# Kernel tuning notes

Hardware: AMD Instinct MI355X
Metric: run time of the kernel (lower is better)

The kernel has to match this reference:

```python
import jax, jax.numpy as jnp
import numpy as np

PENALTY_LAMBDA = 0.5
MAX_RULES = 512
INIT_GATE_LOGIT = -2.0


def setup_inputs() -> dict:
    key = jax.random.key(0)
    k1, k2, k3 = jax.random.split(key, 3)
    B, V, E = 64, 128000, 1000000
    logits = jax.random.normal(k1, (B, V), dtype=jnp.float32)
    # learned per-rule gate logits (nn.Parameter initialized at init_gate_logit;
    # we perturb slightly so gradients are non-degenerate)
    gate_logits = jnp.full((MAX_RULES,), INIT_GATE_LOGIT, dtype=jnp.float32) \
        + 0.1 * jax.random.normal(k2, (MAX_RULES,), dtype=jnp.float32)
    # flattened ragged (rule, token) violation pairs
    kr, kt = jax.random.split(k3)
    rule_ids = jax.random.randint(kr, (E,), 0, MAX_RULES, dtype=jnp.int32)
    token_ids = jax.random.randint(kt, (E,), 0, V, dtype=jnp.int32)
    return {"logits": logits, "gate_logits": gate_logits,
            "rule_ids": rule_ids, "token_ids": token_ids}


def reference(logits, gate_logits, rule_ids, token_ids):
    # eval-mode binary concrete gate (no noise, no thresholding): sigmoid(logit)
    gates = jax.nn.sigmoid(gate_logits)                      # [R]
    V = logits.shape[-1]
    # gated penalty value per (rule, token) pair, single vectorized scatter-add
    vals = gates[rule_ids] * jnp.asarray(PENALTY_LAMBDA, logits.dtype)  # [E]
    pen_1d = jnp.zeros((V,), dtype=logits.dtype).at[token_ids].add(vals)  # [V]
    penalties = jnp.broadcast_to(pen_1d[None, :], logits.shape)           # [B,V]
    modified = logits - penalties
    # coverage loss: -mean of gates over rules that fire (have >=1 violation)
    firing = jnp.zeros((MAX_RULES,), dtype=logits.dtype).at[rule_ids].set(1.0)
    n_firing = jnp.maximum(firing.sum(), 1.0)
    coverage_loss = -(gates * firing).sum() / n_firing
    return modified, coverage_loss, penalties
```

## Files before the change

### kernel.cpp

```cpp
#include <hip/hip_runtime.h>

#define PENALTY_LAMBDA 0.5f
#define RULES 512
#define NR 4
#define RS 32000
#define VOCAB 128000
#define G 64
#define NB 64
#define CH 500
#define CJ 125

typedef float    f32x4 __attribute__((ext_vector_type(4)));
typedef _Float16 f16x4 __attribute__((ext_vector_type(4)));


__global__ void __launch_bounds__(512) scatter_kernel(
    const int* __restrict__ rule_ids, const int* __restrict__ token_ids,
    const float* __restrict__ gate_logits, _Float16* __restrict__ partials,
    unsigned* __restrict__ masks, int E) {
    __shared__ __align__(16) float hist[RS];
    __shared__ float s_g[RULES];
    __shared__ unsigned char s_f[RULES];
    int t = threadIdx.x;
    int g = blockIdx.x;
    int r = blockIdx.y;
    for (int i = t * 4; i < RS; i += 512 * 4)
        *(f32x4*)(hist + i) = (f32x4){0.f, 0.f, 0.f, 0.f};
    if (t < RULES) {
        float x = gate_logits[t];
        s_g[t] = PENALTY_LAMBDA / (1.0f + expf(-x));
    }
    if (t < RULES / 4) ((unsigned*)s_f)[t] = 0u;
    __syncthreads();

    const int lo = r * RS;
    const int stride = G * 512 * 4;
    for (int base = (g * 512 + t) * 4; base + 4 <= E; base += stride) {
        int4 tt = *(const int4*)(token_ids + base);
        int4 rr = *(const int4*)(rule_ids + base);
        int ts[4] = {tt.x, tt.y, tt.z, tt.w};
        int rv[4] = {rr.x, rr.y, rr.z, rr.w};
#pragma unroll
        for (int k = 0; k < 4; ++k) {
            int tok = ts[k] - lo;
            if ((unsigned)tok < (unsigned)RS) atomicAdd(&hist[tok], s_g[rv[k]]);
            if (r == 0) s_f[rv[k]] = 1;
        }
    }
    if (g == 0 && t == 0) {
        for (int e = E & ~3; e < E; ++e) {
            int tok = token_ids[e] - lo; int ru = rule_ids[e];
            if ((unsigned)tok < (unsigned)RS) atomicAdd(&hist[tok], s_g[ru]);
            if (r == 0) s_f[ru] = 1;
        }
    }
    __syncthreads();

    _Float16* dst = partials + ((size_t)r * G + g) * RS;
    for (int i = t * 4; i < RS; i += 512 * 4) {
        f32x4 s = *(const f32x4*)(&hist[i]);
        f16x4 h = {(_Float16)s.x, (_Float16)s.y, (_Float16)s.z, (_Float16)s.w};
        *(f16x4*)(dst + i) = h;
    }

    if (r == 0 && t < 16) {
        const unsigned* w = (const unsigned*)s_f + t * 8;
        unsigned m = 0;
#pragma unroll
        for (int k = 0; k < 8; ++k) {
            unsigned d = w[k];
            if (d & 0x000000FFu) m |= 1u << (k * 4 + 0);
            if (d & 0x0000FF00u) m |= 1u << (k * 4 + 1);
            if (d & 0x00FF0000u) m |= 1u << (k * 4 + 2);
            if (d & 0xFF000000u) m |= 1u << (k * 4 + 3);
        }
        masks[g * 16 + t] = m;
    }
}

__global__ void __launch_bounds__(512) fused_kernel(
    const _Float16* __restrict__ partials, const unsigned* __restrict__ masks,
    const float* __restrict__ gate_logits, const float* __restrict__ logits,
    float* __restrict__ out_mod, float* __restrict__ out_pen,
    float* __restrict__ out_loss) {
    __shared__ float s_pc[CH + 4];
    __shared__ f32x4 s_part[4][CJ + 1];
    int t = threadIdx.x;
    int tx = t & 127, ty = t >> 7;
    int chunk = blockIdx.x;
    int c0 = chunk * CH;
    int r = c0 / RS;
    int bin = c0 - r * RS;

    {
        if (tx < CJ) {
            f32x4 acc = {0.f, 0.f, 0.f, 0.f};
            const _Float16* bp = partials + ((size_t)r * G + ty * 16) * RS
                               + bin + tx * 4;
#pragma unroll 4
            for (int g = 0; g < 16; ++g) {
                f16x4 h = *(const f16x4*)(bp + (size_t)g * RS);
                acc += (f32x4){(float)h.x, (float)h.y, (float)h.z, (float)h.w};
            }
            s_part[ty][tx] = acc;
        } else if (tx == 127) {
            f32x4 e = {0.f, 0.f, 0.f, 0.f};
            for (int i = 0; i < 4; ++i) {
                int gb = c0 + CH + i; if (gb >= VOCAB) gb -= VOCAB;
                int r2 = gb / RS, b2 = gb - r2 * RS;
                const _Float16* bp2 = partials + ((size_t)r2 * G + ty * 16) * RS + b2;
                float s = 0.f;
                for (int g = 0; g < 16; ++g) s += (float)bp2[(size_t)g * RS];
                ((float*)&e)[i] = s;
            }
            s_part[ty][CJ] = e;
        }
    }
    __syncthreads();
    if (t < CJ + 1) {
        f32x4 s = s_part[0][t] + s_part[1][t] + s_part[2][t] + s_part[3][t];
        *(f32x4*)(s_pc + t * 4) = s;
    }
    __syncthreads();

    if (chunk == 0) {
        __shared__ unsigned s_mask[16];
        __shared__ float sg[8], sf[8];
        if (t < 16) {
            unsigned m = 0;
            for (int g = 0; g < G; ++g) m |= masks[g * 16 + t];
            s_mask[t] = m;
        }
        __syncthreads();
        float f = ((s_mask[t >> 5] >> (t & 31)) & 1u) ? 1.f : 0.f;
        float gf = f / (1.f + expf(-gate_logits[t]));
        for (int off = 32; off > 0; off >>= 1) {
            gf += __shfl_down(gf, off, 64);
            f  += __shfl_down(f,  off, 64);
        }
        if ((t & 63) == 0) { sg[t >> 6] = gf; sf[t >> 6] = f; }
        __syncthreads();
        if (t == 0) {
            float tg = 0.f, tf = 0.f;
            for (int w = 0; w < 8; ++w) { tg += sg[w]; tf += sf[w]; }
            *out_loss = -tg / fmaxf(tf, 1.0f);
            out_pen[0] = s_pc[0];
            out_pen[1] = s_pc[1];
            out_pen[2] = s_pc[2];
        }
    }

    if (tx >= CJ) return;
    f32x4 p0 = *(const f32x4*)(s_pc + tx * 4);
    f32x4 ps = {s_pc[tx * 4 + 3], s_pc[tx * 4 + 4],
                s_pc[tx * 4 + 5], s_pc[tx * 4 + 6]};
    bool glast = (chunk == 255 && tx == CJ - 1);
    size_t col = (size_t)c0 + tx * 4;
#pragma unroll 4
    for (int ib = 0; ib < NB / 4; ++ib) {
        int b = ib * 4 + ty;
        size_t base = (size_t)b * VOCAB + col;
        f32x4 l = *(const f32x4*)(logits + base);
        *(f32x4*)(out_mod + base) = l - p0;
        if (glast && b == NB - 1) {
            out_pen[base + 3] = p0.w;
        } else {
            *(f32x4*)(out_pen + base + 3) = ps;
        }
    }
}

extern "C" void kernel_launch(void* const* d_in, const int* in_sizes, int n_in,
                              void* d_out, int out_size, void* d_ws, size_t ws_size,
                              hipStream_t stream) {
    const float* logits      = (const float*)d_in[0];
    const float* gate_logits = (const float*)d_in[1];
    const int*   rule_ids    = (const int*)d_in[2];
    const int*   token_ids   = (const int*)d_in[3];
    float* out = (float*)d_out;

    const int E = in_sizes[2];
    const size_t BV = (size_t)NB * VOCAB;

    _Float16* partials = (_Float16*)d_ws;
    unsigned* masks    = (unsigned*)(partials + (size_t)NR * G * RS);

    scatter_kernel<<<dim3(G, NR), 512, 0, stream>>>(
        rule_ids, token_ids, gate_logits, partials, masks, E);

    fused_kernel<<<VOCAB / CH, 512, 0, stream>>>(
        partials, masks, gate_logits, logits,
        out, out + BV + 1, out + BV);
}
```

Before: 117.9 us.

## Replace per-block LDS histograms with global float atomics into one penalty vector

The partitioned shared-memory histograms and fp16 partial buffers are removed. Instead, a small init kernel zeroes a single 128K-float penalty vector and precomputes the gates, and the scatter kernel applies unsafe (hardware) float atomics straight to that global vector. Rule-firing masks are merged with atomicOr. The fused kernel now reads only the final penalty row, runs on a 2D grid, and uses nontemporal loads and stores. This removes the 32 MB partial write/read and the multi-pass reduction, at the cost of heavy global atomic contention, an extra kernel launch, and a summation order that is no longer deterministic.

New measurement: 160.8 us. 36.4% more time.

```diff
diff --git a/kernel.cpp b/kernel.cpp
--- a/kernel.cpp
+++ b/kernel.cpp
@@ -1,69 +1,56 @@
 #include <hip/hip_runtime.h>
 
-#define PENALTY_LAMBDA 0.5f
 #define RULES 512
-#define NR 4
-#define RS 32000
 #define VOCAB 128000
-#define G 64
 #define NB 64
-#define CH 500
-#define CJ 125
 
-typedef float    f32x4 __attribute__((ext_vector_type(4)));
-typedef _Float16 f16x4 __attribute__((ext_vector_type(4)));
+typedef float f32x4 __attribute__((ext_vector_type(4)));
 
 
-__global__ void __launch_bounds__(512) scatter_kernel(
+__global__ void __launch_bounds__(256) init_kernel(
+    const float* __restrict__ gate_logits, float* __restrict__ pen,
+    unsigned* __restrict__ masks, float* __restrict__ gates) {
+    int t = threadIdx.x, b = blockIdx.x;
+    if (b < VOCAB / 1024) {
+        *(f32x4*)(pen + b * 1024 + t * 4) = (f32x4){0.f, 0.f, 0.f, 0.f};
+    } else {
+        if (t < 16) masks[t] = 0u;
+        float x0 = gate_logits[t], x1 = gate_logits[t + 256];
+        gates[t]       = 0.5f / (1.f + expf(-x0));
+        gates[t + 256] = 0.5f / (1.f + expf(-x1));
+    }
+}
+
+__global__ void __launch_bounds__(256) scatter_kernel(
     const int* __restrict__ rule_ids, const int* __restrict__ token_ids,
-    const float* __restrict__ gate_logits, _Float16* __restrict__ partials,
+    const float* __restrict__ gates, float* __restrict__ pen,
     unsigned* __restrict__ masks, int E) {
-    __shared__ __align__(16) float hist[RS];
     __shared__ float s_g[RULES];
     __shared__ unsigned char s_f[RULES];
     int t = threadIdx.x;
-    int g = blockIdx.x;
-    int r = blockIdx.y;
-    for (int i = t * 4; i < RS; i += 512 * 4)
-        *(f32x4*)(hist + i) = (f32x4){0.f, 0.f, 0.f, 0.f};
-    if (t < RULES) {
-        float x = gate_logits[t];
-        s_g[t] = PENALTY_LAMBDA / (1.0f + expf(-x));
-    }
+    s_g[t] = gates[t];
+    s_g[t + 256] = gates[t + 256];
     if (t < RULES / 4) ((unsigned*)s_f)[t] = 0u;
     __syncthreads();
 
-    const int lo = r * RS;
-    const int stride = G * 512 * 4;
-    for (int base = (g * 512 + t) * 4; base + 4 <= E; base += stride) {
+    const int stride = gridDim.x * 256 * 4;
+    for (int base = (blockIdx.x * 256 + t) * 4; base + 4 <= E; base += stride) {
         int4 tt = *(const int4*)(token_ids + base);
         int4 rr = *(const int4*)(rule_ids + base);
-        int ts[4] = {tt.x, tt.y, tt.z, tt.w};
-        int rv[4] = {rr.x, rr.y, rr.z, rr.w};
-#pragma unroll
-        for (int k = 0; k < 4; ++k) {
-            int tok = ts[k] - lo;
-            if ((unsigned)tok < (unsigned)RS) atomicAdd(&hist[tok], s_g[rv[k]]);
-            if (r == 0) s_f[rv[k]] = 1;
-        }
+        unsafeAtomicAdd(&pen[tt.x], s_g[rr.x]); s_f[rr.x] = 1;
+        unsafeAtomicAdd(&pen[tt.y], s_g[rr.y]); s_f[rr.y] = 1;
+        unsafeAtomicAdd(&pen[tt.z], s_g[rr.z]); s_f[rr.z] = 1;
+        unsafeAtomicAdd(&pen[tt.w], s_g[rr.w]); s_f[rr.w] = 1;
     }
-    if (g == 0 && t == 0) {
+    if (blockIdx.x == 0 && t == 0) {
         for (int e = E & ~3; e < E; ++e) {
-            int tok = token_ids[e] - lo; int ru = rule_ids[e];
-            if ((unsigned)tok < (unsigned)RS) atomicAdd(&hist[tok], s_g[ru]);
-            if (r == 0) s_f[ru] = 1;
+            unsafeAtomicAdd(&pen[token_ids[e]], s_g[rule_ids[e]]);
+            s_f[rule_ids[e]] = 1;
         }
     }
     __syncthreads();
 
-    _Float16* dst = partials + ((size_t)r * G + g) * RS;
-    for (int i = t * 4; i < RS; i += 512 * 4) {
-        f32x4 s = *(const f32x4*)(&hist[i]);
-        f16x4 h = {(_Float16)s.x, (_Float16)s.y, (_Float16)s.z, (_Float16)s.w};
-        *(f16x4*)(dst + i) = h;
-    }
-
-    if (r == 0 && t < 16) {
+    if (t < 16) {
         const unsigned* w = (const unsigned*)s_f + t * 8;
         unsigned m = 0;
 #pragma unroll
@@ -74,98 +61,64 @@
             if (d & 0x00FF0000u) m |= 1u << (k * 4 + 2);
             if (d & 0xFF000000u) m |= 1u << (k * 4 + 3);
         }
-        masks[g * 16 + t] = m;
+        if (m) atomicOr(&masks[t], m);
     }
 }
 
-__global__ void __launch_bounds__(512) fused_kernel(
-    const _Float16* __restrict__ partials, const unsigned* __restrict__ masks,
+__global__ void __launch_bounds__(256) fused_kernel(
+    const float* __restrict__ pen, const unsigned* __restrict__ masks,
     const float* __restrict__ gate_logits, const float* __restrict__ logits,
     float* __restrict__ out_mod, float* __restrict__ out_pen,
     float* __restrict__ out_loss) {
-    __shared__ float s_pc[CH + 4];
-    __shared__ f32x4 s_part[4][CJ + 1];
-    int t = threadIdx.x;
-    int tx = t & 127, ty = t >> 7;
-    int chunk = blockIdx.x;
-    int c0 = chunk * CH;
-    int r = c0 / RS;
-    int bin = c0 - r * RS;
-
-    {
-        if (tx < CJ) {
-            f32x4 acc = {0.f, 0.f, 0.f, 0.f};
-            const _Float16* bp = partials + ((size_t)r * G + ty * 16) * RS
-                               + bin + tx * 4;
-#pragma unroll 4
-            for (int g = 0; g < 16; ++g) {
-                f16x4 h = *(const f16x4*)(bp + (size_t)g * RS);
-                acc += (f32x4){(float)h.x, (float)h.y, (float)h.z, (float)h.w};
-            }
-            s_part[ty][tx] = acc;
-        } else if (tx == 127) {
-            f32x4 e = {0.f, 0.f, 0.f, 0.f};
-            for (int i = 0; i < 4; ++i) {
-                int gb = c0 + CH + i; if (gb >= VOCAB) gb -= VOCAB;
-                int r2 = gb / RS, b2 = gb - r2 * RS;
-                const _Float16* bp2 = partials + ((size_t)r2 * G + ty * 16) * RS + b2;
-                float s = 0.f;
-                for (int g = 0; g < 16; ++g) s += (float)bp2[(size_t)g * RS];
-                ((float*)&e)[i] = s;
-            }
-            s_part[ty][CJ] = e;
+    __shared__ float s_pen[1032];
+    int t = threadIdx.x, bx = blockIdx.x, by = blockIdx.y;
+    int c0 = bx << 10;
+    *(f32x4*)(s_pen + t * 4) = *(const f32x4*)(pen + c0 + t * 4);
+    if (t == 0) {
+#pragma unroll
+        for (int i = 0; i < 4; ++i) {
+            int gc = c0 + 1024 + i; if (gc >= VOCAB) gc -= VOCAB;
+            s_pen[1024 + i] = pen[gc];
         }
     }
     __syncthreads();
-    if (t < CJ + 1) {
-        f32x4 s = s_part[0][t] + s_part[1][t] + s_part[2][t] + s_part[3][t];
-        *(f32x4*)(s_pc + t * 4) = s;
-    }
-    __syncthreads();
 
-    if (chunk == 0) {
-        __shared__ unsigned s_mask[16];
-        __shared__ float sg[8], sf[8];
-        if (t < 16) {
-            unsigned m = 0;
-            for (int g = 0; g < G; ++g) m |= masks[g * 16 + t];
-            s_mask[t] = m;
+    if (bx == 0 && by == 0) {
+        __shared__ float sg[4];
+        float gf = 0.f;
+#pragma unroll
+        for (int k = 0; k < 2; ++k) {
+            int ru = t + k * 256;
+            if ((masks[ru >> 5] >> (ru & 31)) & 1u)
+                gf += 1.f / (1.f + expf(-gate_logits[ru]));
         }
-        __syncthreads();
-        float f = ((s_mask[t >> 5] >> (t & 31)) & 1u) ? 1.f : 0.f;
-        float gf = f / (1.f + expf(-gate_logits[t]));
-        for (int off = 32; off > 0; off >>= 1) {
-            gf += __shfl_down(gf, off, 64);
-            f  += __shfl_down(f,  off, 64);
-        }
-        if ((t & 63) == 0) { sg[t >> 6] = gf; sf[t >> 6] = f; }
+        for (int off = 32; off > 0; off >>= 1) gf += __shfl_down(gf, off, 64);
+        if ((t & 63) == 0) sg[t >> 6] = gf;
         __syncthreads();
         if (t == 0) {
-            float tg = 0.f, tf = 0.f;
-            for (int w = 0; w < 8; ++w) { tg += sg[w]; tf += sf[w]; }
-            *out_loss = -tg / fmaxf(tf, 1.0f);
-            out_pen[0] = s_pc[0];
-            out_pen[1] = s_pc[1];
-            out_pen[2] = s_pc[2];
+            float tf = 0.f;
+#pragma unroll
+            for (int i = 0; i < 16; ++i) tf += (float)__popc(masks[i]);
+            *out_loss = -(sg[0] + sg[1] + sg[2] + sg[3]) / fmaxf(tf, 1.f);
+            out_pen[0] = s_pen[0]; out_pen[1] = s_pen[1]; out_pen[2] = s_pen[2];
         }
     }
 
-    if (tx >= CJ) return;
-    f32x4 p0 = *(const f32x4*)(s_pc + tx * 4);
-    f32x4 ps = {s_pc[tx * 4 + 3], s_pc[tx * 4 + 4],
-                s_pc[tx * 4 + 5], s_pc[tx * 4 + 6]};
-    bool glast = (chunk == 255 && tx == CJ - 1);
-    size_t col = (size_t)c0 + tx * 4;
-#pragma unroll 4
-    for (int ib = 0; ib < NB / 4; ++ib) {
-        int b = ib * 4 + ty;
+    f32x4 p0 = *(const f32x4*)(s_pen + t * 4);
+    f32x4 pn = *(const f32x4*)(s_pen + t * 4 + 4);
+    f32x4 ps = {p0.w, pn.x, pn.y, pn.z};
+    size_t col = (size_t)c0 + t * 4;
+    bool lastcol = (bx == VOCAB / 1024 - 1) && (t == 255);
+#pragma unroll
+    for (int i = 0; i < 8; ++i) {
+        int b = (by << 3) + i;
         size_t base = (size_t)b * VOCAB + col;
-        f32x4 l = *(const f32x4*)(logits + base);
-        *(f32x4*)(out_mod + base) = l - p0;
-        if (glast && b == NB - 1) {
+        f32x4 l = __builtin_nontemporal_load((const f32x4*)(logits + base));
+        __builtin_nontemporal_store(l - p0, (f32x4*)(out_mod + base));
+        if (lastcol && b == NB - 1) {
             out_pen[base + 3] = p0.w;
         } else {
-            *(f32x4*)(out_pen + base + 3) = ps;
+            __builtin_nontemporal_store(ps, (f32x4*)(out_pen + base + 3));
         }
     }
 }
@@ -182,13 +135,12 @@
     const int E = in_sizes[2];
     const size_t BV = (size_t)NB * VOCAB;
 
-    _Float16* partials = (_Float16*)d_ws;
-    unsigned* masks    = (unsigned*)(partials + (size_t)NR * G * RS);
+    float*    pen   = (float*)d_ws;
+    unsigned* masks = (unsigned*)(pen + VOCAB);
+    float*    gates = (float*)(pen + VOCAB + 16);
 
-    scatter_kernel<<<dim3(G, NR), 512, 0, stream>>>(
-        rule_ids, token_ids, gate_logits, partials, masks, E);
-
-    fused_kernel<<<VOCAB / CH, 512, 0, stream>>>(
-        partials, masks, gate_logits, logits,
-        out, out + BV + 1, out + BV);
+    init_kernel<<<VOCAB / 1024 + 1, 256, 0, stream>>>(gate_logits, pen, masks, gates);
+    scatter_kernel<<<1024, 256, 0, stream>>>(rule_ids, token_ids, gates, pen, masks, E);
+    fused_kernel<<<dim3(VOCAB / 1024, NB / 8), 256, 0, stream>>>(
+        pen, masks, gate_logits, logits, out, out + BV + 1, out + BV);
 }
```
